# Performance work log

Hardware: AMD Instinct MI355X
Metric: run time of the kernel (lower is better)

The kernel has to match this reference:

```python
import jax, jax.numpy as jnp
import numpy as np

B, S, D, H = 2, 2048, 1024, 16
HD = D // H
NEG = -10000000000.0

def setup_inputs() -> dict:
    key = jax.random.key(0)
    ks = jax.random.split(key, 9)
    s = 1.0 / np.sqrt(D)
    return {
        "x": jax.random.normal(ks[0], (B, S, D), dtype=jnp.float32),
        "Wq": jax.random.uniform(ks[1], (D, D), jnp.float32, -s, s),
        "bq": jax.random.uniform(ks[2], (D,), jnp.float32, -s, s),
        "Wk": jax.random.uniform(ks[3], (D, D), jnp.float32, -s, s),
        "bk": jax.random.uniform(ks[4], (D,), jnp.float32, -s, s),
        "Wv": jax.random.uniform(ks[5], (D, D), jnp.float32, -s, s),
        "bv": jax.random.uniform(ks[6], (D,), jnp.float32, -s, s),
        "Wo": jax.random.uniform(ks[7], (D, D), jnp.float32, -s, s),
        "bo": jax.random.uniform(ks[8], (D,), jnp.float32, -s, s),
    }

def reference(x, Wq, bq, Wk, bk, Wv, bv, Wo, bo):
    b, s, _ = x.shape
    def split_heads(t):
        return t.reshape(b, s, H, HD).transpose(0, 2, 1, 3)  # [b,h,s,hd]
    Q = split_heads(x @ Wq + bq)
    K = split_heads(x @ Wk + bk)
    V = split_heads(x @ Wv + bv)
    scores = jnp.einsum('bhqd,bhkd->bhqk', Q, K) / jnp.sqrt(jnp.float32(HD))
    causal = jnp.tril(jnp.ones((s, s), dtype=bool))
    scores = jnp.where(causal[None, None], scores, NEG)
    attn = jax.nn.softmax(scores, axis=-1)
    ctx = jnp.einsum('bhqk,bhkd->bhqd', attn, V)
    ctx = ctx.transpose(0, 2, 1, 3).reshape(b, s, D)
    return ctx @ Wo + bo
```

## Files before the change

### kernel.cpp

```cpp
#include <hip/hip_runtime.h>
#include <hip/hip_bf16.h>

#define BB 2
#define SS 2048
#define DD 1024
#define HH 16
#define HD 64
#define MM (BB*SS)

typedef __attribute__((ext_vector_type(8))) short bf16x8;
typedef __attribute__((ext_vector_type(4))) float f32x4;

#define QSCALE 0.18033688f

static __device__ __forceinline__ unsigned short f2bf(float f) {
    unsigned int u = __builtin_bit_cast(unsigned int, f);
    u += 0x7fffu + ((u >> 16) & 1u);
    return (unsigned short)(u >> 16);
}

static __device__ __forceinline__ void gload16(const unsigned short* g, unsigned short* l) {
    __builtin_amdgcn_global_load_lds(
        (const __attribute__((address_space(1))) unsigned int*)g,
        (__attribute__((address_space(3))) unsigned int*)l, 16, 0, 0);
}

__global__ __launch_bounds__(256) void prep_kernel(const float* __restrict__ x,
                                                   const float* __restrict__ W0,
                                                   const float* __restrict__ W1,
                                                   const float* __restrict__ W2,
                                                   const float* __restrict__ W3,
                                                   unsigned short* __restrict__ xb,
                                                   unsigned short* __restrict__ Wt)
{
    const int t = threadIdx.x;
    const int bid = blockIdx.x;
    if (bid < 2048) {
        const size_t i = ((size_t)bid * 256 + t) * 8;
        float4 a = *(const float4*)(x + i);
        float4 b = *(const float4*)(x + i + 4);
        union { unsigned short u[8]; bf16x8 v; } pk;
        pk.u[0] = f2bf(a.x); pk.u[1] = f2bf(a.y); pk.u[2] = f2bf(a.z); pk.u[3] = f2bf(a.w);
        pk.u[4] = f2bf(b.x); pk.u[5] = f2bf(b.y); pk.u[6] = f2bf(b.z); pk.u[7] = f2bf(b.w);
        *(bf16x8*)(xb + i) = pk.v;
        return;
    }
    __shared__ unsigned short Ts[64][72];
    const int wsel = (bid - 2048) >> 8;
    const int rem  = (bid - 2048) & 255;
    const float* W = wsel == 0 ? W0 : wsel == 1 ? W1 : wsel == 2 ? W2 : W3;
    unsigned short* out = Wt + (size_t)wsel * DD * DD;
    const int n0 = (rem & 15) * 64, k0 = (rem >> 4) * 64;
#pragma unroll
    for (int i = 0; i < 4; ++i) {
        const int r = (t >> 4) + i * 16;
        const int c = (t & 15) * 4;
        float4 v = *(const float4*)(W + (size_t)(k0 + r) * DD + n0 + c);
        Ts[c + 0][r] = f2bf(v.x); Ts[c + 1][r] = f2bf(v.y);
        Ts[c + 2][r] = f2bf(v.z); Ts[c + 3][r] = f2bf(v.w);
    }
    __syncthreads();
#pragma unroll
    for (int j = 0; j < 2; ++j) {
        const int ch = j * 256 + t;
        const int rn = ch >> 3, ck = (ch & 7) * 8;
        bf16x8 v = *(const bf16x8*)&Ts[rn][ck];
        *(bf16x8*)(out + (size_t)(n0 + rn) * DD + k0 + ck) = v;
    }
}

__global__ __launch_bounds__(256) void gemm_mfma(const unsigned short* __restrict__ A,
                                                 const unsigned short* __restrict__ Bt,
                                                 const float* __restrict__ bias0,
                                                 const float* __restrict__ bias1,
                                                 const float* __restrict__ bias2,
                                                 unsigned short* __restrict__ Qb,
                                                 unsigned short* __restrict__ Kb,
                                                 unsigned short* __restrict__ Vb,
                                                 float* __restrict__ outf,
                                                 int mode)
{
    __shared__ unsigned short As[2][128 * 64];
    __shared__ unsigned short Bs[2][128 * 64];

    const int t = threadIdx.x;
    const int w = t >> 6, l = t & 63;
    const int lane16 = l & 15, quad = l >> 4;
    const int m0 = blockIdx.x * 128, n0 = blockIdx.y * 128;
    const int wm = (w & 1) * 64, wn = (w >> 1) * 64;

    f32x4 acc[4][4] = {};

    int srow[4], skcg[4];
#pragma unroll
    for (int j = 0; j < 4; ++j) {
        const int c = t + j * 256;
        srow[j] = c >> 3;
        skcg[j] = (c & 7) ^ (srow[j] & 7);
    }

#pragma unroll
    for (int j = 0; j < 4; ++j) {
        const int c = t + j * 256;
        gload16(A  + (size_t)(m0 + srow[j]) * DD + skcg[j] * 8, &As[0][c * 8]);
        gload16(Bt + (size_t)(n0 + srow[j]) * DD + skcg[j] * 8, &Bs[0][c * 8]);
    }
    __syncthreads();

#pragma unroll 2
    for (int kt = 0; kt < 16; ++kt) {
        const int cur = kt & 1;
        if (kt + 1 < 16) {
            const int k1 = (kt + 1) * 64;
#pragma unroll
            for (int j = 0; j < 4; ++j) {
                const int c = t + j * 256;
                gload16(A  + (size_t)(m0 + srow[j]) * DD + k1 + skcg[j] * 8, &As[cur ^ 1][c * 8]);
                gload16(Bt + (size_t)(n0 + srow[j]) * DD + k1 + skcg[j] * 8, &Bs[cur ^ 1][c * 8]);
            }
        }
#pragma unroll
        for (int h = 0; h < 2; ++h) {
            bf16x8 af[4], bfr[4];
#pragma unroll
            for (int mt = 0; mt < 4; ++mt) {
                const int row = wm + mt * 16 + lane16;
                af[mt] = *(const bf16x8*)&As[cur][(row * 8 + ((h * 4 + quad) ^ (row & 7))) * 8];
            }
#pragma unroll
            for (int nt = 0; nt < 4; ++nt) {
                const int row = wn + nt * 16 + lane16;
                bfr[nt] = *(const bf16x8*)&Bs[cur][(row * 8 + ((h * 4 + quad) ^ (row & 7))) * 8];
            }
#pragma unroll
            for (int mt = 0; mt < 4; ++mt)
#pragma unroll
                for (int nt = 0; nt < 4; ++nt)
                    acc[mt][nt] = __builtin_amdgcn_mfma_f32_16x16x32_bf16(af[mt], bfr[nt], acc[mt][nt], 0, 0, 0);
        }
        __syncthreads();
    }

    if (mode == 0) {
        const int which = n0 >> 10;
        const float* bias = which == 0 ? bias0 : which == 1 ? bias1 : bias2;
#pragma unroll
        for (int nt = 0; nt < 4; ++nt) {
            const int gcol = n0 + wn + nt * 16 + lane16;
            const int cd = gcol & 1023;
            const float bv = bias[cd];
            const int h_ = cd >> 6, d = cd & 63;
            if (which == 2) {
#pragma unroll
                for (int mt = 0; mt < 4; ++mt) {
                    const int row0 = m0 + wm + mt * 16 + quad * 4;
                    const int b_ = row0 >> 11, s0 = row0 & 2047;
                    union { unsigned short u[4]; uint2 v; } pk;
#pragma unroll
                    for (int r = 0; r < 4; ++r) pk.u[r] = f2bf(acc[mt][nt][r] + bv);
                    *(uint2*)(Vb + ((size_t)(b_ * HH + h_) * HD + d) * SS + s0) = pk.v;
                }
            } else {
                unsigned short* dst3 = which == 0 ? Qb : Kb;
                const float sc_ = which == 0 ? QSCALE : 1.0f;
#pragma unroll
                for (int mt = 0; mt < 4; ++mt)
#pragma unroll
                    for (int r = 0; r < 4; ++r) {
                        const int row = m0 + wm + mt * 16 + quad * 4 + r;
                        const int b_ = row >> 11, s_ = row & 2047;
                        dst3[(((size_t)(b_ * HH + h_) * SS + s_) * HD) + d] =
                            f2bf((acc[mt][nt][r] + bv) * sc_);
                    }
            }
        }
    } else {
#pragma unroll
        for (int nt = 0; nt < 4; ++nt) {
            const int gcol = n0 + wn + nt * 16 + lane16;
            const float bv = bias0[gcol];
#pragma unroll
            for (int mt = 0; mt < 4; ++mt)
#pragma unroll
                for (int r = 0; r < 4; ++r) {
                    const int row = m0 + wm + mt * 16 + quad * 4 + r;
                    outf[(size_t)row * DD + gcol] = acc[mt][nt][r] + bv;
                }
        }
    }
}

__global__ __launch_bounds__(512) void attn_mfma(const unsigned short* __restrict__ Q,
                                                 const unsigned short* __restrict__ K,
                                                 const unsigned short* __restrict__ V,
                                                 unsigned short* __restrict__ ctx)
{
    __shared__ unsigned short Ks[2][4096];
    __shared__ unsigned short Vs[2][4096];
    __shared__ unsigned short Ps[8][1280];

    const int t = threadIdx.x;
    const int w = t >> 6, l = t & 63;
    const int lane16 = l & 15, quad = l >> 4;
    const int bid = blockIdx.x;
    const int halfg = bid >> 8, idx = bid & 255;
    const int qb_ = idx >> 5;
    const int qblk = halfg ? qb_ : 15 - qb_;
    const int hb = idx & 31;
    const int h = hb & 15, b = hb >> 4;
    const int q0 = qblk * 128;
    const size_t bh = (size_t)(b * HH + h) * SS;
    const unsigned short* Vg = V + (size_t)(b * HH + h) * HD * SS;

    const int wrow0 = q0 + w * 16;
    bf16x8 qf0 = *(const bf16x8*)(Q + (bh + wrow0 + lane16) * HD + quad * 8);
    bf16x8 qf1 = *(const bf16x8*)(Q + (bh + wrow0 + lane16) * HD + 32 + quad * 8);

    f32x4 Oc[4] = {};
    float lpart[4] = {};

    const int ntiles = 2 * qblk + 2;
    const int sr = t >> 3;
    const int sg = (t & 7) ^ (sr & 7);

    {
        gload16(K  + (bh + sr) * HD + sg * 8, &Ks[0][t * 8]);
        gload16(Vg + (size_t)sr * SS + sg * 8, &Vs[0][t * 8]);
    }

    for (int kt = 0; kt < ntiles; ++kt) {
        __syncthreads();
        if (kt + 1 < ntiles) {
            const int k1 = (kt + 1) * 64;
            const int bi = (kt + 1) & 1;
            gload16(K  + (bh + k1 + sr) * HD + sg * 8, &Ks[bi][t * 8]);
            gload16(Vg + (size_t)sr * SS + k1 + sg * 8, &Vs[bi][t * 8]);
        }
        const int k0 = kt * 64;
        if (k0 > wrow0 + 15) continue;
        const unsigned short* Kt = Ks[kt & 1];
        const unsigned short* Vt = Vs[kt & 1];

        f32x4 sc[4] = {};
#pragma unroll
        for (int nt = 0; nt < 4; ++nt) {
            const int row = nt * 16 + lane16;
            bf16x8 k0f = *(const bf16x8*)&Kt[(row * 8 + (quad ^ (row & 7))) * 8];
            bf16x8 k1f = *(const bf16x8*)&Kt[(row * 8 + ((4 + quad) ^ (row & 7))) * 8];
            sc[nt] = __builtin_amdgcn_mfma_f32_16x16x32_bf16(qf0, k0f, sc[nt], 0, 0, 0);
            sc[nt] = __builtin_amdgcn_mfma_f32_16x16x32_bf16(qf1, k1f, sc[nt], 0, 0, 0);
        }

        float pr[4][4];
        if (k0 + 63 > wrow0) {
#pragma unroll
            for (int r = 0; r < 4; ++r) {
                const int row = wrow0 + quad * 4 + r;
#pragma unroll
                for (int nt = 0; nt < 4; ++nt)
                    if (k0 + nt * 16 + lane16 > row) sc[nt][r] = -1e30f;
            }
        }
#pragma unroll
        for (int nt = 0; nt < 4; ++nt)
#pragma unroll
            for (int r = 0; r < 4; ++r) pr[nt][r] = __builtin_amdgcn_exp2f(sc[nt][r]);
#pragma unroll
        for (int r = 0; r < 4; ++r)
            lpart[r] += (pr[0][r] + pr[1][r]) + (pr[2][r] + pr[3][r]);

        unsigned short* Pw = Ps[w];
#pragma unroll
        for (int nt = 0; nt < 4; ++nt) {
            const int plane = (nt >> 1) * 640, colin = (nt & 1) * 16 + lane16;
#pragma unroll
            for (int r = 0; r < 4; ++r)
                Pw[plane + (quad * 4 + r) * 40 + colin] = f2bf(pr[nt][r]);
        }
        bf16x8 pf0 = *(const bf16x8*)&Pw[lane16 * 40 + quad * 8];
        bf16x8 pf1 = *(const bf16x8*)&Pw[640 + lane16 * 40 + quad * 8];

#pragma unroll
        for (int dt = 0; dt < 4; ++dt) {
            const int drow = dt * 16 + lane16;
            bf16x8 v0 = *(const bf16x8*)&Vt[(drow * 8 + (quad ^ (drow & 7))) * 8];
            bf16x8 v1 = *(const bf16x8*)&Vt[(drow * 8 + ((4 + quad) ^ (drow & 7))) * 8];
            Oc[dt] = __builtin_amdgcn_mfma_f32_16x16x32_bf16(pf0, v0, Oc[dt], 0, 0, 0);
            Oc[dt] = __builtin_amdgcn_mfma_f32_16x16x32_bf16(pf1, v1, Oc[dt], 0, 0, 0);
        }
    }

#pragma unroll
    for (int off = 1; off < 16; off <<= 1)
#pragma unroll
        for (int r = 0; r < 4; ++r) lpart[r] += __shfl_xor(lpart[r], off);

#pragma unroll
    for (int r = 0; r < 4; ++r) {
        const float inv = 1.f / lpart[r];
        const int row = wrow0 + quad * 4 + r;
        unsigned short* dst = ctx + ((size_t)(b * SS) + row) * DD + h * HD + lane16;
#pragma unroll
        for (int dt = 0; dt < 4; ++dt) dst[dt * 16] = f2bf(Oc[dt][r] * inv);
    }
}

extern "C" void kernel_launch(void* const* d_in, const int* in_sizes, int n_in,
                              void* d_out, int out_size, void* d_ws, size_t ws_size,
                              hipStream_t stream) {
    const float* x  = (const float*)d_in[0];
    const float* Wq = (const float*)d_in[1];
    const float* bq = (const float*)d_in[2];
    const float* Wk = (const float*)d_in[3];
    const float* bk = (const float*)d_in[4];
    const float* Wv = (const float*)d_in[5];
    const float* bv = (const float*)d_in[6];
    const float* Wo = (const float*)d_in[7];
    const float* bo = (const float*)d_in[8];
    float* out = (float*)d_out;

    unsigned short* xb  = (unsigned short*)d_ws;
    unsigned short* Wt  = xb  + (size_t)MM * DD;
    unsigned short* Qb  = Wt  + (size_t)4 * DD * DD;
    unsigned short* Kb  = Qb  + (size_t)MM * DD;
    unsigned short* Vb  = Kb  + (size_t)MM * DD;
    unsigned short* ctxb = Vb + (size_t)MM * DD;

    prep_kernel<<<2048 + 1024, 256, 0, stream>>>(x, Wq, Wk, Wv, Wo, xb, Wt);

    gemm_mfma<<<dim3(MM / 128, 3072 / 128), 256, 0, stream>>>(
        xb, Wt, bq, bk, bv, Qb, Kb, Vb, nullptr, 0);

    attn_mfma<<<(SS / 128) * HH * BB, 512, 0, stream>>>(Qb, Kb, Vb, ctxb);

    gemm_mfma<<<dim3(MM / 128, DD / 128), 256, 0, stream>>>(
        ctxb, Wt + (size_t)3 * DD * DD, bo, nullptr, nullptr,
        nullptr, nullptr, nullptr, out, 1);
}
```

Before: 190.1 us.

## Rewrite attention with 32x32 MFMA, register-resident P via permlane swaps

The attention kernel now uses 4 waves (256 threads), each owning 32 query rows, and computes S^T = K·Q^T with 32x32x16 bf16 MFMAs. The P matrix is no longer staged through shared memory: the probabilities are packed to bf16 with v_cvt_pk_bf16_f32 and rearranged across lane halves with v_permlane32_swap so they can feed the P·V MFMA directly, which removes the LDS writes, reads and the Ps buffer. K/V tile loads are split across twice as many loads per thread. The cost is a larger register footprint per wave and fewer waves per block, which may lower latency hiding.

Result: no change. 190.2 us (+0.1%).

```diff
diff --git a/kernel.cpp b/kernel.cpp
--- a/kernel.cpp
+++ b/kernel.cpp
@@ -10,6 +10,7 @@
 
 typedef __attribute__((ext_vector_type(8))) short bf16x8;
 typedef __attribute__((ext_vector_type(4))) float f32x4;
+typedef __attribute__((ext_vector_type(16))) float f32x16;
 
 #define QSCALE 0.18033688f
 
@@ -190,18 +191,17 @@
     }
 }
 
-__global__ __launch_bounds__(512) void attn_mfma(const unsigned short* __restrict__ Q,
+__global__ __launch_bounds__(256) void attn_mfma(const unsigned short* __restrict__ Q,
                                                  const unsigned short* __restrict__ K,
                                                  const unsigned short* __restrict__ V,
                                                  unsigned short* __restrict__ ctx)
 {
     __shared__ unsigned short Ks[2][4096];
     __shared__ unsigned short Vs[2][4096];
-    __shared__ unsigned short Ps[8][1280];
 
     const int t = threadIdx.x;
     const int w = t >> 6, l = t & 63;
-    const int lane16 = l & 15, quad = l >> 4;
+    const int l31 = l & 31, hi = l >> 5;
     const int bid = blockIdx.x;
     const int halfg = bid >> 8, idx = bid & 255;
     const int qb_ = idx >> 5;
@@ -212,20 +212,24 @@
     const size_t bh = (size_t)(b * HH + h) * SS;
     const unsigned short* Vg = V + (size_t)(b * HH + h) * HD * SS;
 
-    const int wrow0 = q0 + w * 16;
-    bf16x8 qf0 = *(const bf16x8*)(Q + (bh + wrow0 + lane16) * HD + quad * 8);
-    bf16x8 qf1 = *(const bf16x8*)(Q + (bh + wrow0 + lane16) * HD + 32 + quad * 8);
-
-    f32x4 Oc[4] = {};
-    float lpart[4] = {};
+    const int wq0 = q0 + w * 32;
+    bf16x8 qf[4];
+#pragma unroll
+    for (int dt = 0; dt < 4; ++dt)
+        qf[dt] = *(const bf16x8*)(Q + (bh + wq0 + l31) * HD + dt * 16 + hi * 8);
+
+    f32x16 ot[2] = {};
+    float lp = 0.f;
 
     const int ntiles = 2 * qblk + 2;
-    const int sr = t >> 3;
-    const int sg = (t & 7) ^ (sr & 7);
+    const int sr0 = t >> 3,          sg0 = (t & 7) ^ (sr0 & 7);
+    const int sr1 = (t + 256) >> 3,  sg1 = ((t + 256) & 7) ^ (sr1 & 7);
 
     {
-        gload16(K  + (bh + sr) * HD + sg * 8, &Ks[0][t * 8]);
-        gload16(Vg + (size_t)sr * SS + sg * 8, &Vs[0][t * 8]);
+        gload16(K  + (bh + sr0) * HD + sg0 * 8,        &Ks[0][t * 8]);
+        gload16(K  + (bh + sr1) * HD + sg1 * 8,        &Ks[0][(t + 256) * 8]);
+        gload16(Vg + (size_t)sr0 * SS + sg0 * 8,       &Vs[0][t * 8]);
+        gload16(Vg + (size_t)sr1 * SS + sg1 * 8,       &Vs[0][(t + 256) * 8]);
     }
 
     for (int kt = 0; kt < ntiles; ++kt) {
@@ -233,76 +237,88 @@
         if (kt + 1 < ntiles) {
             const int k1 = (kt + 1) * 64;
             const int bi = (kt + 1) & 1;
-            gload16(K  + (bh + k1 + sr) * HD + sg * 8, &Ks[bi][t * 8]);
-            gload16(Vg + (size_t)sr * SS + k1 + sg * 8, &Vs[bi][t * 8]);
+            gload16(K  + (bh + k1 + sr0) * HD + sg0 * 8,   &Ks[bi][t * 8]);
+            gload16(K  + (bh + k1 + sr1) * HD + sg1 * 8,   &Ks[bi][(t + 256) * 8]);
+            gload16(Vg + (size_t)sr0 * SS + k1 + sg0 * 8,  &Vs[bi][t * 8]);
+            gload16(Vg + (size_t)sr1 * SS + k1 + sg1 * 8,  &Vs[bi][(t + 256) * 8]);
         }
         const int k0 = kt * 64;
-        if (k0 > wrow0 + 15) continue;
+        if (k0 > wq0 + 31) continue;
         const unsigned short* Kt = Ks[kt & 1];
         const unsigned short* Vt = Vs[kt & 1];
 
-        f32x4 sc[4] = {};
-#pragma unroll
-        for (int nt = 0; nt < 4; ++nt) {
-            const int row = nt * 16 + lane16;
-            bf16x8 k0f = *(const bf16x8*)&Kt[(row * 8 + (quad ^ (row & 7))) * 8];
-            bf16x8 k1f = *(const bf16x8*)&Kt[(row * 8 + ((4 + quad) ^ (row & 7))) * 8];
-            sc[nt] = __builtin_amdgcn_mfma_f32_16x16x32_bf16(qf0, k0f, sc[nt], 0, 0, 0);
-            sc[nt] = __builtin_amdgcn_mfma_f32_16x16x32_bf16(qf1, k1f, sc[nt], 0, 0, 0);
-        }
-
-        float pr[4][4];
-        if (k0 + 63 > wrow0) {
-#pragma unroll
-            for (int r = 0; r < 4; ++r) {
-                const int row = wrow0 + quad * 4 + r;
-#pragma unroll
-                for (int nt = 0; nt < 4; ++nt)
-                    if (k0 + nt * 16 + lane16 > row) sc[nt][r] = -1e30f;
-            }
-        }
-#pragma unroll
-        for (int nt = 0; nt < 4; ++nt)
-#pragma unroll
-            for (int r = 0; r < 4; ++r) pr[nt][r] = __builtin_amdgcn_exp2f(sc[nt][r]);
-#pragma unroll
-        for (int r = 0; r < 4; ++r)
-            lpart[r] += (pr[0][r] + pr[1][r]) + (pr[2][r] + pr[3][r]);
-
-        unsigned short* Pw = Ps[w];
-#pragma unroll
-        for (int nt = 0; nt < 4; ++nt) {
-            const int plane = (nt >> 1) * 640, colin = (nt & 1) * 16 + lane16;
-#pragma unroll
-            for (int r = 0; r < 4; ++r)
-                Pw[plane + (quad * 4 + r) * 40 + colin] = f2bf(pr[nt][r]);
-        }
-        bf16x8 pf0 = *(const bf16x8*)&Pw[lane16 * 40 + quad * 8];
-        bf16x8 pf1 = *(const bf16x8*)&Pw[640 + lane16 * 40 + quad * 8];
-
+        f32x16 s[2] = {};
 #pragma unroll
         for (int dt = 0; dt < 4; ++dt) {
-            const int drow = dt * 16 + lane16;
-            bf16x8 v0 = *(const bf16x8*)&Vt[(drow * 8 + (quad ^ (drow & 7))) * 8];
-            bf16x8 v1 = *(const bf16x8*)&Vt[(drow * 8 + ((4 + quad) ^ (drow & 7))) * 8];
-            Oc[dt] = __builtin_amdgcn_mfma_f32_16x16x32_bf16(pf0, v0, Oc[dt], 0, 0, 0);
-            Oc[dt] = __builtin_amdgcn_mfma_f32_16x16x32_bf16(pf1, v1, Oc[dt], 0, 0, 0);
-        }
-    }
-
-#pragma unroll
-    for (int off = 1; off < 16; off <<= 1)
-#pragma unroll
-        for (int r = 0; r < 4; ++r) lpart[r] += __shfl_xor(lpart[r], off);
-
-#pragma unroll
-    for (int r = 0; r < 4; ++r) {
-        const float inv = 1.f / lpart[r];
-        const int row = wrow0 + quad * 4 + r;
-        unsigned short* dst = ctx + ((size_t)(b * SS) + row) * DD + h * HD + lane16;
-#pragma unroll
-        for (int dt = 0; dt < 4; ++dt) dst[dt * 16] = f2bf(Oc[dt][r] * inv);
-    }
+#pragma unroll
+            for (int kh = 0; kh < 2; ++kh) {
+                const int row = kh * 32 + l31;
+                bf16x8 kf = *(const bf16x8*)&Kt[(row * 8 + ((dt * 2 + hi) ^ (row & 7))) * 8];
+                s[kh] = __builtin_amdgcn_mfma_f32_32x32x16_bf16(kf, qf[dt], s[kh], 0, 0, 0);
+            }
+        }
+
+        if (k0 + 63 > wq0) {
+            const int q = wq0 + l31;
+#pragma unroll
+            for (int kh = 0; kh < 2; ++kh)
+#pragma unroll
+                for (int r = 0; r < 16; ++r) {
+                    const int k = k0 + kh * 32 + (r & 3) + 8 * (r >> 2) + 4 * hi;
+                    if (k > q) s[kh][r] = -1e30f;
+                }
+        }
+
+#pragma unroll
+        for (int kh = 0; kh < 2; ++kh) {
+#pragma unroll
+            for (int r = 0; r < 16; ++r) s[kh][r] = __builtin_amdgcn_exp2f(s[kh][r]);
+            const float t0 = (s[kh][0] + s[kh][1]) + (s[kh][2] + s[kh][3]);
+            const float t1 = (s[kh][4] + s[kh][5]) + (s[kh][6] + s[kh][7]);
+            const float t2 = (s[kh][8] + s[kh][9]) + (s[kh][10] + s[kh][11]);
+            const float t3 = (s[kh][12] + s[kh][13]) + (s[kh][14] + s[kh][15]);
+            lp += (t0 + t1) + (t2 + t3);
+        }
+
+#pragma unroll
+        for (int kh = 0; kh < 2; ++kh) {
+#pragma unroll
+            for (int c = 0; c < 2; ++c) {
+                const int rb = c * 8;
+                unsigned int w0, w1, w2, w3;
+                asm("v_cvt_pk_bf16_f32 %0, %1, %2" : "=v"(w0) : "v"(s[kh][rb + 0]), "v"(s[kh][rb + 1]));
+                asm("v_cvt_pk_bf16_f32 %0, %1, %2" : "=v"(w2) : "v"(s[kh][rb + 4]), "v"(s[kh][rb + 5]));
+                asm("v_cvt_pk_bf16_f32 %0, %1, %2" : "=v"(w1) : "v"(s[kh][rb + 2]), "v"(s[kh][rb + 3]));
+                asm("v_cvt_pk_bf16_f32 %0, %1, %2" : "=v"(w3) : "v"(s[kh][rb + 6]), "v"(s[kh][rb + 7]));
+                asm("v_permlane32_swap_b32 %0, %1" : "+v"(w0), "+v"(w2));
+                asm("v_permlane32_swap_b32 %0, %1" : "+v"(w1), "+v"(w3));
+                union { unsigned int u[4]; bf16x8 v; } pa;
+                pa.u[0] = w0; pa.u[1] = w1; pa.u[2] = w2; pa.u[3] = w3;
+                const int chunk = kh * 4 + c * 2 + hi;
+                const int rlo = l31, rhi2 = 32 + l31;
+                bf16x8 v0 = *(const bf16x8*)&Vt[(rlo * 8 + (chunk ^ (rlo & 7))) * 8];
+                bf16x8 v1 = *(const bf16x8*)&Vt[(rhi2 * 8 + (chunk ^ (rhi2 & 7))) * 8];
+                ot[0] = __builtin_amdgcn_mfma_f32_32x32x16_bf16(v0, pa.v, ot[0], 0, 0, 0);
+                ot[1] = __builtin_amdgcn_mfma_f32_32x32x16_bf16(v1, pa.v, ot[1], 0, 0, 0);
+            }
+        }
+    }
+
+    lp += __shfl_xor(lp, 32);
+    const float inv = 1.f / lp;
+
+    const int qrow = wq0 + l31;
+    unsigned short* dst = ctx + ((size_t)(b * SS) + qrow) * DD + h * HD;
+#pragma unroll
+    for (int a2 = 0; a2 < 2; ++a2)
+#pragma unroll
+        for (int u = 0; u < 4; ++u) {
+            const int d0 = a2 * 32 + 8 * u + 4 * hi;
+            union { unsigned short u4[4]; uint2 v; } pk;
+#pragma unroll
+            for (int r = 0; r < 4; ++r) pk.u4[r] = f2bf(ot[a2][4 * u + r] * inv);
+            *(uint2*)(dst + d0) = pk.v;
+        }
 }
 
 extern "C" void kernel_launch(void* const* d_in, const int* in_sizes, int n_in,
@@ -331,7 +347,7 @@
     gemm_mfma<<<dim3(MM / 128, 3072 / 128), 256, 0, stream>>>(
         xb, Wt, bq, bk, bv, Qb, Kb, Vb, nullptr, 0);
 
-    attn_mfma<<<(SS / 128) * HH * BB, 512, 0, stream>>>(Qb, Kb, Vb, ctxb);
+    attn_mfma<<<(SS / 128) * HH * BB, 256, 0, stream>>>(Qb, Kb, Vb, ctxb);
 
     gemm_mfma<<<dim3(MM / 128, DD / 128), 256, 0, stream>>>(
         ctxb, Wt + (size_t)3 * DD * DD, bo, nullptr, nullptr,
```
